# Kernel optimization log

Measured on AMD Instinct MI355X. Metric: run time of the kernel, lower is better.

## Reference

```python
import jax, jax.numpy as jnp
import numpy as np

MIN_NEAR = 0.05
DENSITY_SCALE = 1.0
BOUND = 1.0  # spherical scene bounds radius
GEO = 15


def _density_mlp(x, dW1, db1, dW2, db2, dW3, db3):
    h = jax.nn.relu(x @ dW1 + db1)
    h = jax.nn.relu(h @ dW2 + db2)
    h = h @ dW3 + db3  # [M, 1+GEO]
    sigma = jnp.exp(jnp.clip(h[..., 0], -15.0, 15.0))  # trunc_exp
    return sigma, h[..., 1:]


def _color_mlp(d, geo, cW1, cb1, cW2, cb2, cW3, cb3):
    h = jnp.concatenate([d, geo], axis=-1)
    h = jax.nn.relu(h @ cW1 + cb1)
    h = jax.nn.relu(h @ cW2 + cb2)
    return jax.nn.sigmoid(h @ cW3 + cb3)


def _comp_weights(deltas, sigmas):
    # alpha compositing: w_i = alpha_i * prod_{j<i}(1 - alpha_j)
    alphas = 1.0 - jnp.exp(-deltas * sigmas)
    trans = jnp.cumprod(
        jnp.concatenate([jnp.ones_like(alphas[:, :1]), 1.0 - alphas + 1e-15], axis=-1),
        axis=-1)[:, :-1]
    return alphas * trans


def _sample_pdf(bins, weights, n_samples):
    # deterministic importance resampling (eval mode); bins [N,T-1], weights [N,T-2]
    weights = weights + 1e-5
    pdf = weights / jnp.sum(weights, axis=-1, keepdims=True)
    cdf = jnp.cumsum(pdf, axis=-1)
    cdf = jnp.concatenate([jnp.zeros_like(cdf[:, :1]), cdf], axis=-1)  # [N, T-1]
    u = jnp.linspace(0.5 / n_samples, 1.0 - 0.5 / n_samples, n_samples)
    u = jnp.broadcast_to(u, (bins.shape[0], n_samples))
    inds = jax.vmap(lambda c, uu: jnp.searchsorted(c, uu, side='right'))(cdf, u)
    below = jnp.clip(inds - 1, 0, cdf.shape[-1] - 1)
    above = jnp.clip(inds, 0, cdf.shape[-1] - 1)
    cdf_g0 = jnp.take_along_axis(cdf, below, axis=-1)
    cdf_g1 = jnp.take_along_axis(cdf, above, axis=-1)
    bmax = bins.shape[-1] - 1
    bins_g0 = jnp.take_along_axis(bins, jnp.clip(below, 0, bmax), axis=-1)
    bins_g1 = jnp.take_along_axis(bins, jnp.clip(above, 0, bmax), axis=-1)
    denom = jnp.where(cdf_g1 - cdf_g0 < 1e-5, 1.0, cdf_g1 - cdf_g0)
    t = (u - cdf_g0) / denom
    return bins_g0 + t * (bins_g1 - bins_g0)


def _run(rays_o, rays_d, dW1, db1, dW2, db2, dW3, db3,
         cW1, cb1, cW2, cb2, cW3, cb3, num_steps, upsample_steps):
    N = rays_o.shape[0]
    # get_z_val_bounds: ray/sphere intersection, sphere radius BOUND at origin
    b = jnp.sum(rays_o * rays_d, axis=-1)
    c = jnp.sum(rays_o * rays_o, axis=-1) - BOUND ** 2
    disc = jnp.maximum(b * b - c, 0.0)
    z_max = jnp.maximum(-b + jnp.sqrt(disc), MIN_NEAR + 1e-3)
    z_min = jnp.full_like(z_max, MIN_NEAR)
    # get_foreground_z_vals: per-ray linspace (perturb=False)
    t = jnp.linspace(0.0, 1.0, num_steps)
    z_vals = z_min[:, None] + (z_max - z_min)[:, None] * t[None, :]
    z_vals = jnp.clip(z_vals, z_min[:, None], z_max[:, None])
    xyzs = rays_o[:, None, :] + rays_d[:, None, :] * z_vals[..., None]
    sigma, geo = _density_mlp(xyzs.reshape(-1, 3), dW1, db1, dW2, db2, dW3, db3)
    sigma = sigma.reshape(N, num_steps)
    geo = geo.reshape(N, num_steps, GEO)

    # upsample_z_values: importance resampling from coarse weights
    deltas = z_vals[:, 1:] - z_vals[:, :-1]
    aug = jnp.concatenate([deltas, deltas[:, -1:]], axis=-1)
    w_coarse = _comp_weights(aug, DENSITY_SCALE * sigma)
    z_mid = 0.5 * (z_vals[:, :-1] + z_vals[:, 1:])
    new_z = jax.lax.stop_gradient(_sample_pdf(z_mid, w_coarse[:, 1:-1], upsample_steps))
    new_xyzs = rays_o[:, None, :] + rays_d[:, None, :] * new_z[..., None]
    new_sigma, new_geo = _density_mlp(new_xyzs.reshape(-1, 3), dW1, db1, dW2, db2, dW3, db3)
    new_sigma = new_sigma.reshape(N, upsample_steps)
    new_geo = new_geo.reshape(N, upsample_steps, GEO)

    # sort/gather merge of coarse + fine samples
    z_all = jnp.concatenate([z_vals, new_z], axis=1)
    order = jnp.argsort(z_all, axis=1)
    z_vals = jnp.take_along_axis(z_all, order, axis=1)  # [N, T]
    xyzs = jnp.take_along_axis(jnp.concatenate([xyzs, new_xyzs], axis=1), order[..., None], axis=1)
    sigma = jnp.take_along_axis(jnp.concatenate([sigma, new_sigma], axis=1), order, axis=1)
    geo = jnp.take_along_axis(jnp.concatenate([geo, new_geo], axis=1), order[..., None], axis=1)

    deltas = z_vals[:, 1:] - z_vals[:, :-1]
    aug = jnp.concatenate([deltas, deltas[:, -1:]], axis=-1)
    weights = _comp_weights(aug, DENSITY_SCALE * sigma)  # [N, T]

    mask = weights > 1e-4
    dirs = jnp.broadcast_to(rays_d[:, None, :], xyzs.shape).reshape(-1, 3)
    rgb = _color_mlp(dirs, geo.reshape(-1, GEO), cW1, cb1, cW2, cb2, cW3, cb3)
    rgbs = jnp.where(mask.reshape(-1, 1), rgb, 0.0).reshape(N, -1, 3)

    weights_sum = jnp.sum(weights, axis=-1)
    depth = jnp.sum(weights * z_vals, axis=-1)
    image = jnp.sum(weights[..., None] * rgbs, axis=-2)
    bg = 206.0 / 255.0
    image = image + (1.0 - weights_sum)[..., None] * bg

    # pairwise distortion loss (the (z_shifted - z_shifted) term in the source is identically zero)
    sample_dist = 1.0 / num_steps
    z_shift = jnp.concatenate([z_vals[:, 1:], jnp.full((N, 1), sample_dist, z_vals.dtype)], axis=-1)
    mid_zs = 0.5 * z_vals + 0.5 * z_shift
    pair = jnp.abs(mid_zs[:, None, :] - mid_zs[:, :, None]) * (weights[:, None, :] * weights[:, :, None])
    loss = jnp.sum(pair, axis=(1, 2)) / (depth + 1e-6)
    loss = jnp.where(loss < 1e-3, 0.0, loss)  # cutoff
    return jnp.concatenate([image, depth[:, None], loss[:, None]], axis=-1)  # [N, 5]


def setup_inputs() -> dict:
    key = jax.random.key(0)
    ks = jax.random.split(key, 16)
    N, H = 2048, 256
    rays_o = 0.1 * jax.random.normal(ks[0], (N, 3), jnp.float32)  # near scene centre
    rd = jax.random.normal(ks[1], (N, 3), jnp.float32)
    rays_d = rd / jnp.linalg.norm(rd, axis=-1, keepdims=True)

    def w(k, shape):
        return jax.random.normal(k, shape, jnp.float32) * (1.0 / np.sqrt(shape[0]))

    return {
        'rays_o': rays_o, 'rays_d': rays_d,
        'dW1': w(ks[2], (3, H)), 'db1': jnp.zeros(H, jnp.float32),
        'dW2': w(ks[3], (H, H)), 'db2': jnp.zeros(H, jnp.float32),
        'dW3': w(ks[4], (H, 1 + GEO)), 'db3': jnp.zeros(1 + GEO, jnp.float32),
        'cW1': w(ks[5], (3 + GEO, H)), 'cb1': jnp.zeros(H, jnp.float32),
        'cW2': w(ks[6], (H, H)), 'cb2': jnp.zeros(H, jnp.float32),
        'cW3': w(ks[7], (H, 3)), 'cb3': jnp.zeros(3, jnp.float32),
        'num_steps': 128, 'upsample_steps': 128,
    }


def reference(rays_o, rays_d, dW1, db1, dW2, db2, dW3, db3,
              cW1, cb1, cW2, cb2, cW3, cb3, num_steps, upsample_steps):
    return _run(rays_o, rays_d, dW1, db1, dW2, db2, dW3, db3,
                cW1, cb1, cW2, cb2, cW3, cb3, num_steps, upsample_steps)
```

## Files before the change

kernel.cpp:

```cpp
#include <hip/hip_runtime.h>


typedef float f32x4 __attribute__((ext_vector_type(4)));
typedef __bf16 bf16x8 __attribute__((ext_vector_type(8)));
typedef unsigned short u16x8 __attribute__((ext_vector_type(8)));
typedef unsigned short u16x4 __attribute__((ext_vector_type(4)));

#define NRAYS 2048
#define NSTEP 128
#define TSAMP 256
#define MIN_NEAR 0.05f
#define DTPW 4
#define CTPW 4

__device__ __forceinline__ unsigned short f2bf(float f) {
  unsigned int u = __float_as_uint(f);
  u += 0x7FFFu + ((u >> 16) & 1u);
  return (unsigned short)(u >> 16);
}

__global__ void k_pack(const float* __restrict__ W, unsigned short* __restrict__ dst,
                       int K, int Norig, int NT, int total) {
  int idx = blockIdx.x * 256 + threadIdx.x;
  if (idx >= total) return;
  int per = NT * 512;
  int kt = idx / per;
  int rm = idx % per;
  int nt = rm >> 9;
  int lane = (rm >> 3) & 63;
  int j = rm & 7;
  int k = kt * 32 + ((lane >> 4) << 3) + j;
  int n = nt * 16 + (lane & 15);
  float v = (k < K && n < Norig) ? W[k * Norig + n] : 0.0f;
  dst[idx] = f2bf(v);
}

__global__ void k_pack_d3(const float* __restrict__ dW3, unsigned short* __restrict__ dst) {
  int idx = blockIdx.x * 256 + threadIdx.x;
  int lane = (idx >> 3) & 63;
  int j = idx & 7;
  int kt = idx >> 9;
  int k = kt * 32 + ((lane >> 4) << 3) + j;
  int n = lane & 15;
  dst[idx] = f2bf(dW3[k * 16 + ((n + 1) & 15)]);
}

__global__ void k_pack_c1(const float* __restrict__ cW1, unsigned short* __restrict__ dst) {
  int idx = blockIdx.x * 256 + threadIdx.x;
  int nt = idx >> 9;
  int lane = (idx >> 3) & 63;
  int j = idx & 7;
  int k = ((lane >> 4) << 3) + j;
  int n = nt * 16 + (lane & 15);
  float v = 0.0f;
  if (k < 15) v = cW1[(3 + k) * 256 + n];
  else if (k >= 16 && k < 19) v = cW1[(k - 16) * 256 + n];
  dst[idx] = f2bf(v);
}

__global__ void k_raysetup(const float* __restrict__ o, const float* __restrict__ d,
                           float* __restrict__ z_c) {
  int r = blockIdx.x, i = threadIdx.x;
  float ox = o[r * 3], oy = o[r * 3 + 1], oz = o[r * 3 + 2];
  float dx = d[r * 3], dy = d[r * 3 + 1], dz = d[r * 3 + 2];
  float b = ox * dx + oy * dy + oz * dz;
  float c = ox * ox + oy * oy + oz * oz - 1.0f;
  float disc = fmaxf(b * b - c, 0.0f);
  float zmax = fmaxf(-b + sqrtf(disc), MIN_NEAR + 1e-3f);
  float zmin = MIN_NEAR;
  float t = (float)i / 127.0f;
  float z = zmin + (zmax - zmin) * t;
  z = fminf(fmaxf(z, zmin), zmax);
  z_c[r * NSTEP + i] = z;
}


__device__ __forceinline__ void mlp_l1(const unsigned short* xb, unsigned short* buf,
                                       const bf16x8 (&w1r)[4], const float* sb1,
                                       int wid, int quad, int col) {
#pragma unroll
  for (int h = 0; h < 2; ++h) {
    f32x4 acc[8];
#pragma unroll
    for (int i = 0; i < 8; ++i) acc[i] = (f32x4){0.f, 0.f, 0.f, 0.f};
    int p0 = (h * 2) * 16 + col, p1 = (h * 2 + 1) * 16 + col;
    bf16x8 x0 = *reinterpret_cast<const bf16x8*>(&xb[p0 * 32 + ((quad ^ (p0 & 3)) * 8)]);
    bf16x8 x1 = *reinterpret_cast<const bf16x8*>(&xb[p1 * 32 + ((quad ^ (p1 & 3)) * 8)]);
#pragma unroll
    for (int ntl = 0; ntl < 4; ++ntl) {
      acc[ntl * 2 + 0] = __builtin_amdgcn_mfma_f32_16x16x32_bf16(w1r[ntl], x0, acc[ntl * 2 + 0], 0, 0, 0);
      acc[ntl * 2 + 1] = __builtin_amdgcn_mfma_f32_16x16x32_bf16(w1r[ntl], x1, acc[ntl * 2 + 1], 0, 0, 0);
    }
#pragma unroll
    for (int ntl = 0; ntl < 4; ++ntl) {
      int n = (wid * 4 + ntl) * 16 + quad * 4;
      f32x4 bv = *reinterpret_cast<const f32x4*>(&sb1[n]);
#pragma unroll
      for (int j = 0; j < 2; ++j) {
        int p = (h * 2 + j) * 16 + col;
        u16x4 pk;
#pragma unroll
        for (int rr = 0; rr < 4; ++rr)
          pk[rr] = f2bf(fmaxf(acc[ntl * 2 + j][rr] + bv[rr], 0.0f));
        *reinterpret_cast<u16x4*>(&buf[p * 256 + (((n >> 3) ^ (p & 31)) * 8) + (n & 7)]) = pk;
      }
    }
  }
}

__device__ __forceinline__ void l2_half_compute(const unsigned short* buf,
                                                const bf16x8 (&w2r)[8][4],
                                                f32x4 (&acc)[8], int h, int quad, int col) {
#pragma unroll
  for (int i = 0; i < 8; ++i) acc[i] = (f32x4){0.f, 0.f, 0.f, 0.f};
#pragma unroll
  for (int kt = 0; kt < 8; ++kt) {
    int p0 = (h * 2) * 16 + col, p1 = (h * 2 + 1) * 16 + col;
    bf16x8 x0 = *reinterpret_cast<const bf16x8*>(&buf[p0 * 256 + (((kt * 4 + quad) ^ (p0 & 31)) * 8)]);
    bf16x8 x1 = *reinterpret_cast<const bf16x8*>(&buf[p1 * 256 + (((kt * 4 + quad) ^ (p1 & 31)) * 8)]);
#pragma unroll
    for (int ntl = 0; ntl < 4; ++ntl) {
      acc[ntl * 2 + 0] = __builtin_amdgcn_mfma_f32_16x16x32_bf16(w2r[kt][ntl], x0, acc[ntl * 2 + 0], 0, 0, 0);
      acc[ntl * 2 + 1] = __builtin_amdgcn_mfma_f32_16x16x32_bf16(w2r[kt][ntl], x1, acc[ntl * 2 + 1], 0, 0, 0);
    }
  }
}

__device__ __forceinline__ void l2_half_write(unsigned short* buf, const f32x4 (&acc)[8],
                                              const float* sb2, int h, int wid, int quad, int col) {
#pragma unroll
  for (int ntl = 0; ntl < 4; ++ntl) {
    int n = (wid * 4 + ntl) * 16 + quad * 4;
    f32x4 bv = *reinterpret_cast<const f32x4*>(&sb2[n]);
#pragma unroll
    for (int j = 0; j < 2; ++j) {
      int p = (h * 2 + j) * 16 + col;
      u16x4 pk;
#pragma unroll
      for (int rr = 0; rr < 4; ++rr)
        pk[rr] = f2bf(fmaxf(acc[ntl * 2 + j][rr] + bv[rr], 0.0f));
      *reinterpret_cast<u16x4*>(&buf[p * 256 + (((n >> 3) ^ (p & 31)) * 8) + (n & 7)]) = pk;
    }
  }
}

__global__ __launch_bounds__(256, 2)
void k_density(const float* __restrict__ rays_o, const float* __restrict__ rays_d,
               const float* __restrict__ z,
               const unsigned short* __restrict__ Wp1, const float* __restrict__ b1,
               const unsigned short* __restrict__ Wp2, const float* __restrict__ b2,
               const unsigned short* __restrict__ Wp3, const float* __restrict__ b3,
               unsigned short* __restrict__ gout, float* __restrict__ sig) {
  __shared__ unsigned short buf[64 * 256];
  __shared__ unsigned short xb[64 * 32];
  __shared__ unsigned short sW3[4096];
  __shared__ __align__(16) float sb1[256];
  __shared__ __align__(16) float sb2[256];
  __shared__ float sb3[16];
  const int t = threadIdx.x;
  const int lane = t & 63, wid = t >> 6, quad = lane >> 4, col = lane & 15;
  const int p_ = t >> 2, g_ = t & 3;

  sb1[t] = b1[t];
  sb2[t] = b2[t];
  if (t < 16) sb3[t] = b3[(t + 1) & 15];
  { const u16x8* s = (const u16x8*)Wp3; u16x8* d = (u16x8*)sW3;
    d[t] = s[t]; d[t + 256] = s[t + 256]; }

  bf16x8 w1r[4], w2r[8][4];
#pragma unroll
  for (int ntl = 0; ntl < 4; ++ntl)
    w1r[ntl] = *reinterpret_cast<const bf16x8*>(Wp1 + ((wid * 4 + ntl) * 64 + lane) * 8);
#pragma unroll
  for (int kt = 0; kt < 8; ++kt)
#pragma unroll
    for (int ntl = 0; ntl < 4; ++ntl)
      w2r[kt][ntl] = *reinterpret_cast<const bf16x8*>(Wp2 + ((kt * 16 + wid * 4 + ntl) * 64 + lane) * 8);

  float zv = z[blockIdx.x * DTPW * 64 + p_];

#pragma unroll 1
  for (int tt = 0; tt < DTPW; ++tt) {
    const int P0 = (blockIdx.x * DTPW + tt) * 64;
    {
      u16x8 pk = {0, 0, 0, 0, 0, 0, 0, 0};
      if (g_ == 0) {
        int r = (P0 + p_) >> 7;
        pk[0] = f2bf(rays_o[r * 3 + 0] + rays_d[r * 3 + 0] * zv);
        pk[1] = f2bf(rays_o[r * 3 + 1] + rays_d[r * 3 + 1] * zv);
        pk[2] = f2bf(rays_o[r * 3 + 2] + rays_d[r * 3 + 2] * zv);
      }
      *reinterpret_cast<u16x8*>(&xb[p_ * 32 + ((g_ ^ (p_ & 3)) * 8)]) = pk;
    }
    __syncthreads();
    mlp_l1(xb, buf, w1r, sb1, wid, quad, col);
    __syncthreads();
    float zn = 0.0f;
    if (tt + 1 < DTPW) zn = z[P0 + 64 + p_];
    f32x4 acc[8];
    l2_half_compute(buf, w2r, acc, 0, quad, col);
    __syncthreads();
    l2_half_write(buf, acc, sb2, 0, wid, quad, col);
    l2_half_compute(buf, w2r, acc, 1, quad, col);
    __syncthreads();
    l2_half_write(buf, acc, sb2, 1, wid, quad, col);
    __syncthreads();
    {
      const int p = wid * 16 + col;
      f32x4 a3 = {0.f, 0.f, 0.f, 0.f};
#pragma unroll
      for (int kt = 0; kt < 8; ++kt) {
        bf16x8 w = *reinterpret_cast<const bf16x8*>(&sW3[(kt * 64 + lane) * 8]);
        bf16x8 x = *reinterpret_cast<const bf16x8*>(&buf[p * 256 + (((kt * 4 + quad) ^ (p & 31)) * 8)]);
        a3 = __builtin_amdgcn_mfma_f32_16x16x32_bf16(w, x, a3, 0, 0, 0);
      }
      int n0 = quad * 4;
      u16x4 pk;
#pragma unroll
      for (int rr = 0; rr < 4; ++rr) {
        float v = a3[rr] + sb3[n0 + rr];
        if (quad == 3 && rr == 3) {
          sig[P0 + p] = expf(fminf(fmaxf(v, -15.f), 15.f));
          pk[rr] = 0;
        } else {
          pk[rr] = f2bf(v);
        }
      }
      *reinterpret_cast<u16x4*>(gout + (size_t)(P0 + p) * 16 + n0) = pk;
    }
    zv = zn;
  }
}

__global__ void k_pdf(const float* __restrict__ z_c, const float* __restrict__ sigc,
                      float* __restrict__ z_f) {
  __shared__ float sz[128], sl[128], sw[128], scdf[128], szmid[128];
  int r = blockIdx.x, i = threadIdx.x;
  float zi = z_c[r * NSTEP + i];
  sz[i] = zi;
  float sg = sigc[r * NSTEP + i];
  __syncthreads();
  float aug = (i < 127) ? (sz[i + 1] - zi) : (sz[127] - sz[126]);
  float alpha = 1.0f - expf(-aug * sg);
  float term = 1.0f - alpha + 1e-15f;
  sl[i] = logf(term);
  __syncthreads();
  for (int off = 1; off < 128; off <<= 1) {
    float y = (i >= off) ? sl[i - off] : 0.0f;
    __syncthreads();
    sl[i] += y;
    __syncthreads();
  }
  float excl = (i > 0) ? sl[i - 1] : 0.0f;
  float w = alpha * expf(excl);
  sw[i] = w;
  __syncthreads();
  float v = (i < 126) ? (sw[i + 1] + 1e-5f) : 0.0f;
  sl[i] = v;
  __syncthreads();
  for (int off = 1; off < 128; off <<= 1) {
    float y = (i >= off) ? sl[i - off] : 0.0f;
    __syncthreads();
    sl[i] += y;
    __syncthreads();
  }
  float total = sl[125];
  if (i <= 126) scdf[i] = (i == 0) ? 0.0f : sl[i - 1] / total;
  if (i < 127) szmid[i] = 0.5f * (sz[i] + sz[i + 1]);
  __syncthreads();
  const float lo = 0.5f / 128.0f, hi = 1.0f - 0.5f / 128.0f;
  float u = lo + (hi - lo) * ((float)i / 127.0f);
  int loI = 0, hiI = 127;
  while (loI < hiI) {
    int mid = (loI + hiI) >> 1;
    if (scdf[mid] > u) hiI = mid; else loI = mid + 1;
  }
  int inds = loI;
  int below = inds - 1; if (below < 0) below = 0; if (below > 126) below = 126;
  int above = inds; if (above > 126) above = 126;
  float c0 = scdf[below], c1 = scdf[above];
  float b0 = szmid[below], b1 = szmid[above];
  float dn = c1 - c0; if (dn < 1e-5f) dn = 1.0f;
  float tt = (u - c0) / dn;
  z_f[r * NSTEP + i] = b0 + tt * (b1 - b0);
}

__global__ void k_merge(const float* __restrict__ z_c, const float* __restrict__ z_f,
                        const float* __restrict__ sigc, const float* __restrict__ sigf,
                        float* __restrict__ z_m, int* __restrict__ order,
                        float* __restrict__ wgt) {
  __shared__ float szc[128], szf[128], szm[256], sl[256];
  __shared__ int sord[256];
  int r = blockIdx.x, t = threadIdx.x;
  if (t < 128) szc[t] = z_c[r * NSTEP + t];
  else szf[t - 128] = z_f[r * NSTEP + t - 128];
  __syncthreads();
  int pos; float myz;
  if (t < 128) {
    myz = szc[t];
    int lo = 0, hi = 128;
    while (lo < hi) { int m = (lo + hi) >> 1; if (szf[m] < myz) lo = m + 1; else hi = m; }
    pos = t + lo;
  } else {
    int j = t - 128; myz = szf[j];
    int lo = 0, hi = 128;
    while (lo < hi) { int m = (lo + hi) >> 1; if (szc[m] <= myz) lo = m + 1; else hi = m; }
    pos = j + lo;
  }
  szm[pos] = myz; sord[pos] = t;
  __syncthreads();
  z_m[r * TSAMP + t] = szm[t];
  order[r * TSAMP + t] = sord[t];
  int src = sord[t];
  float sg = (src < 128) ? sigc[r * NSTEP + src] : sigf[r * NSTEP + (src - 128)];
  float zt = szm[t];
  float aug = (t < 255) ? (szm[t + 1] - zt) : (szm[255] - szm[254]);
  float alpha = 1.0f - expf(-aug * sg);
  sl[t] = logf(1.0f - alpha + 1e-15f);
  __syncthreads();
  for (int off = 1; off < 256; off <<= 1) {
    float y = (t >= off) ? sl[t - off] : 0.0f;
    __syncthreads();
    sl[t] += y;
    __syncthreads();
  }
  float excl = (t > 0) ? sl[t - 1] : 0.0f;
  wgt[r * TSAMP + t] = alpha * expf(excl);
}

__global__ __launch_bounds__(256, 2)
void k_color(const float* __restrict__ rays_d, const int* __restrict__ order,
             const float* __restrict__ wgt,
             const unsigned short* __restrict__ goutc, const unsigned short* __restrict__ goutf,
             const unsigned short* __restrict__ Wp1, const float* __restrict__ cb1,
             const unsigned short* __restrict__ Wp2, const float* __restrict__ cb2,
             const unsigned short* __restrict__ Wp3, const float* __restrict__ cb3,
             float* __restrict__ rgb4) {
  __shared__ unsigned short buf[64 * 256];
  __shared__ unsigned short xb[64 * 32];
  __shared__ unsigned short sW3[4096];
  __shared__ __align__(16) float sb1[256];
  __shared__ __align__(16) float sb2[256];
  const int t = threadIdx.x;
  const int lane = t & 63, wid = t >> 6, quad = lane >> 4, col = lane & 15;
  const int p_ = t >> 2, g_ = t & 3;

  sb1[t] = cb1[t];
  sb2[t] = cb2[t];
  { const u16x8* s = (const u16x8*)Wp3; u16x8* d = (u16x8*)sW3;
    d[t] = s[t]; d[t + 256] = s[t + 256]; }

  bf16x8 w1r[4], w2r[8][4];
#pragma unroll
  for (int ntl = 0; ntl < 4; ++ntl)
    w1r[ntl] = *reinterpret_cast<const bf16x8*>(Wp1 + ((wid * 4 + ntl) * 64 + lane) * 8);
#pragma unroll
  for (int kt = 0; kt < 8; ++kt)
#pragma unroll
    for (int ntl = 0; ntl < 4; ++ntl)
      w2r[kt][ntl] = *reinterpret_cast<const bf16x8*>(Wp2 + ((kt * 16 + wid * 4 + ntl) * 64 + lane) * 8);

  u16x8 gx = {0, 0, 0, 0, 0, 0, 0, 0};
  float wgtv = 0.0f;
  {
    int P = blockIdx.x * CTPW * 64 + p_;
    int r = P >> 8;
    if (g_ < 2) {
      int src = order[P];
      const unsigned short* gs = (src < 128)
          ? (goutc + (size_t)(r * NSTEP + src) * 16)
          : (goutf + (size_t)(r * NSTEP + (src - 128)) * 16);
      gx = *reinterpret_cast<const u16x8*>(gs + g_ * 8);
    } else if (g_ == 2) {
      gx[0] = f2bf(rays_d[r * 3 + 0]);
      gx[1] = f2bf(rays_d[r * 3 + 1]);
      gx[2] = f2bf(rays_d[r * 3 + 2]);
    } else {
      wgtv = wgt[P];
    }
  }

#pragma unroll 1
  for (int tt = 0; tt < CTPW; ++tt) {
    const int P0 = (blockIdx.x * CTPW + tt) * 64;
    const int haveNext = (tt + 1 < CTPW);
    int go = __syncthreads_or((g_ == 3) && (wgtv > 1e-4f));
    int ordn = 0; float wgtn = 0.0f;
    u16x8 gxn = {0, 0, 0, 0, 0, 0, 0, 0};
    if (go) {
      *reinterpret_cast<u16x8*>(&xb[p_ * 32 + ((g_ ^ (p_ & 3)) * 8)]) = gx;
      __syncthreads();
      mlp_l1(xb, buf, w1r, sb1, wid, quad, col);
      __syncthreads();
    }
    if (haveNext) {
      int Pn = P0 + 64 + p_;
      int rn = Pn >> 8;
      if (g_ < 2) ordn = order[Pn];
      else if (g_ == 2) {
        gxn[0] = f2bf(rays_d[rn * 3 + 0]);
        gxn[1] = f2bf(rays_d[rn * 3 + 1]);
        gxn[2] = f2bf(rays_d[rn * 3 + 2]);
      } else wgtn = wgt[Pn];
    }
    f32x4 acc[8];
    if (go) {
      l2_half_compute(buf, w2r, acc, 0, quad, col);
      __syncthreads();
      l2_half_write(buf, acc, sb2, 0, wid, quad, col);
    }
    if (haveNext && g_ < 2) {
      int Pn = P0 + 64 + p_;
      int rn = Pn >> 8;
      const unsigned short* gs = (ordn < 128)
          ? (goutc + (size_t)(rn * NSTEP + ordn) * 16)
          : (goutf + (size_t)(rn * NSTEP + (ordn - 128)) * 16);
      gxn = *reinterpret_cast<const u16x8*>(gs + g_ * 8);
    }
    if (go) {
      l2_half_compute(buf, w2r, acc, 1, quad, col);
      __syncthreads();
      l2_half_write(buf, acc, sb2, 1, wid, quad, col);
      __syncthreads();
      {
        const int p = wid * 16 + col;
        f32x4 a3 = {0.f, 0.f, 0.f, 0.f};
#pragma unroll
        for (int kt = 0; kt < 8; ++kt) {
          bf16x8 w = *reinterpret_cast<const bf16x8*>(&sW3[(kt * 64 + lane) * 8]);
          bf16x8 x = *reinterpret_cast<const bf16x8*>(&buf[p * 256 + (((kt * 4 + quad) ^ (p & 31)) * 8)]);
          a3 = __builtin_amdgcn_mfma_f32_16x16x32_bf16(w, x, a3, 0, 0, 0);
        }
        if (quad == 0) {
          f32x4 v;
#pragma unroll
          for (int rr = 0; rr < 3; ++rr) {
            float s = a3[rr] + cb3[rr];
            v[rr] = 1.0f / (1.0f + expf(-s));
          }
          v[3] = 0.0f;
          *reinterpret_cast<f32x4*>(rgb4 + (size_t)(P0 + p) * 4) = v;
        }
      }
    }
    gx = gxn; wgtv = wgtn;
  }
}

__device__ __forceinline__ float block_reduce(float v, float* s, int t) {
  s[t] = v;
  __syncthreads();
  for (int off = 128; off > 0; off >>= 1) {
    if (t < off) s[t] += s[t + off];
    __syncthreads();
  }
  float r = s[0];
  __syncthreads();
  return r;
}

__global__ void k_final(const float* __restrict__ z_m, const float* __restrict__ wgt,
                        const float* __restrict__ rgb4, float* __restrict__ out) {
  __shared__ float sz[256], sw[256], smid[256], sred[256];
  int r = blockIdx.x, t = threadIdx.x;
  float zt = z_m[r * TSAMP + t];
  float wt = wgt[r * TSAMP + t];
  sz[t] = zt; sw[t] = wt;
  __syncthreads();
  float znext = (t < 255) ? sz[t + 1] : (1.0f / 128.0f);
  smid[t] = 0.5f * zt + 0.5f * znext;
  float cr = 0.f, cg = 0.f, cb = 0.f;
  if (wt > 1e-4f) {
    f32x4 c = *reinterpret_cast<const f32x4*>(rgb4 + (size_t)(r * TSAMP + t) * 4);
    cr = c[0]; cg = c[1]; cb = c[2];
  }
  __syncthreads();
  float mt = smid[t];
  float acc = 0.f;
  for (int j = 0; j < 256; ++j) acc += fabsf(mt - smid[j]) * sw[j];
  acc *= wt;
  float wsum = block_reduce(wt, sred, t);
  float depth = block_reduce(wt * zt, sred, t);
  float ir = block_reduce(wt * cr, sred, t);
  float ig = block_reduce(wt * cg, sred, t);
  float ib = block_reduce(wt * cb, sred, t);
  float S = block_reduce(acc, sred, t);
  if (t == 0) {
    const float bgc = 206.0f / 255.0f;
    float loss = S / (depth + 1e-6f);
    if (loss < 1e-3f) loss = 0.0f;
    out[r * 5 + 0] = ir + (1.0f - wsum) * bgc;
    out[r * 5 + 1] = ig + (1.0f - wsum) * bgc;
    out[r * 5 + 2] = ib + (1.0f - wsum) * bgc;
    out[r * 5 + 3] = depth;
    out[r * 5 + 4] = loss;
  }
}

extern "C" void kernel_launch(void* const* d_in, const int* in_sizes, int n_in,
                              void* d_out, int out_size, void* d_ws, size_t ws_size,
                              hipStream_t stream) {
  const float* rays_o = (const float*)d_in[0];
  const float* rays_d = (const float*)d_in[1];
  const float* dW1 = (const float*)d_in[2];
  const float* db1 = (const float*)d_in[3];
  const float* dW2 = (const float*)d_in[4];
  const float* db2 = (const float*)d_in[5];
  const float* dW3 = (const float*)d_in[6];
  const float* db3 = (const float*)d_in[7];
  const float* cW1 = (const float*)d_in[8];
  const float* cb1 = (const float*)d_in[9];
  const float* cW2 = (const float*)d_in[10];
  const float* cb2 = (const float*)d_in[11];
  const float* cW3 = (const float*)d_in[12];
  const float* cb3 = (const float*)d_in[13];

  char* ws = (char*)d_ws;
  size_t off = 0;
  auto alloc = [&](size_t bytes) -> void* {
    void* p = ws + off;
    off += (bytes + 255) & ~(size_t)255;
    return p;
  };
  unsigned short* Wp_d1 = (unsigned short*)alloc(8192 * 2);
  unsigned short* Wp_d2 = (unsigned short*)alloc(65536 * 2);
  unsigned short* Wp_d3 = (unsigned short*)alloc(4096 * 2);
  unsigned short* Wp_c1 = (unsigned short*)alloc(8192 * 2);
  unsigned short* Wp_c2 = (unsigned short*)alloc(65536 * 2);
  unsigned short* Wp_c3 = (unsigned short*)alloc(4096 * 2);
  float* z_c  = (float*)alloc((size_t)NRAYS * NSTEP * 4);
  float* z_f  = (float*)alloc((size_t)NRAYS * NSTEP * 4);
  unsigned short* goutc = (unsigned short*)alloc((size_t)NRAYS * NSTEP * 16 * 2);
  unsigned short* goutf = (unsigned short*)alloc((size_t)NRAYS * NSTEP * 16 * 2);
  float* sigc = (float*)alloc((size_t)NRAYS * NSTEP * 4);
  float* sigf = (float*)alloc((size_t)NRAYS * NSTEP * 4);
  float* z_m  = (float*)alloc((size_t)NRAYS * TSAMP * 4);
  int*   ordr = (int*)alloc((size_t)NRAYS * TSAMP * 4);
  float* wgt  = (float*)alloc((size_t)NRAYS * TSAMP * 4);
  float* rgb4 = (float*)alloc((size_t)NRAYS * TSAMP * 4 * 4);
  (void)ws_size; (void)in_sizes; (void)n_in; (void)out_size;

  k_pack<<<8192 / 256, 256, 0, stream>>>(dW1, Wp_d1, 3, 256, 16, 8192);
  k_pack<<<65536 / 256, 256, 0, stream>>>(dW2, Wp_d2, 256, 256, 16, 65536);
  k_pack_d3<<<4096 / 256, 256, 0, stream>>>(dW3, Wp_d3);
  k_pack_c1<<<8192 / 256, 256, 0, stream>>>(cW1, Wp_c1);
  k_pack<<<65536 / 256, 256, 0, stream>>>(cW2, Wp_c2, 256, 256, 16, 65536);
  k_pack<<<4096 / 256, 256, 0, stream>>>(cW3, Wp_c3, 256, 3, 1, 4096);

  k_raysetup<<<NRAYS, 128, 0, stream>>>(rays_o, rays_d, z_c);
  k_density<<<(NRAYS * NSTEP) / (64 * DTPW), 256, 0, stream>>>(
      rays_o, rays_d, z_c, Wp_d1, db1, Wp_d2, db2, Wp_d3, db3, goutc, sigc);
  k_pdf<<<NRAYS, 128, 0, stream>>>(z_c, sigc, z_f);
  k_density<<<(NRAYS * NSTEP) / (64 * DTPW), 256, 0, stream>>>(
      rays_o, rays_d, z_f, Wp_d1, db1, Wp_d2, db2, Wp_d3, db3, goutf, sigf);
  k_merge<<<NRAYS, 256, 0, stream>>>(z_c, z_f, sigc, sigf, z_m, ordr, wgt);
  k_color<<<(NRAYS * TSAMP) / (64 * CTPW), 256, 0, stream>>>(
      rays_d, ordr, wgt, goutc, goutf, Wp_c1, cb1, Wp_c2, cb2, Wp_c3, cb3, rgb4);
  k_final<<<NRAYS, 256, 0, stream>>>(z_m, wgt, rgb4, (float*)d_out);
}
```

Baseline: 308.9 us.

## Fuse pack, raysetup, pdf, merge, color and final passes into fewer kernels

Merges the six weight-pack kernels into one launch and computes the coarse z values inline instead of in a separate setup kernel. The PDF resampling now runs at the end of the first density pass, since each 256-point block covers exactly two rays. Merge, color MLP and final compositing become one per-ray kernel that keeps order, weights and rgb in shared memory rather than global memory. This cuts launches and global round-trips, but the color kernel now runs with one ray per block, loads its weights into registers per ray, and uses more shared memory, which may lower occupancy.

```diff
diff --git a/kernel.cpp b/kernel.cpp
--- a/kernel.cpp
+++ b/kernel.cpp
@@ -3,6 +3,7 @@
 
 typedef float f32x4 __attribute__((ext_vector_type(4)));
 typedef __bf16 bf16x8 __attribute__((ext_vector_type(8)));
+typedef __bf16 bf16x4 __attribute__((ext_vector_type(4)));
 typedef unsigned short u16x8 __attribute__((ext_vector_type(8)));
 typedef unsigned short u16x4 __attribute__((ext_vector_type(4)));
 
@@ -11,67 +12,80 @@
 #define TSAMP 256
 #define MIN_NEAR 0.05f
 #define DTPW 4
-#define CTPW 4
+
+#define OFF_D1 0
+#define OFF_D2 8192
+#define OFF_D3 73728
+#define OFF_C1 77824
+#define OFF_C2 86016
+#define OFF_C3 151552
+#define PACK_TOTAL 155648
 
 __device__ __forceinline__ unsigned short f2bf(float f) {
-  unsigned int u = __float_as_uint(f);
-  u += 0x7FFFu + ((u >> 16) & 1u);
-  return (unsigned short)(u >> 16);
-}
-
-__global__ void k_pack(const float* __restrict__ W, unsigned short* __restrict__ dst,
-                       int K, int Norig, int NT, int total) {
-  int idx = blockIdx.x * 256 + threadIdx.x;
-  if (idx >= total) return;
-  int per = NT * 512;
-  int kt = idx / per;
-  int rm = idx % per;
-  int nt = rm >> 9;
-  int lane = (rm >> 3) & 63;
-  int j = rm & 7;
-  int k = kt * 32 + ((lane >> 4) << 3) + j;
-  int n = nt * 16 + (lane & 15);
-  float v = (k < K && n < Norig) ? W[k * Norig + n] : 0.0f;
-  dst[idx] = f2bf(v);
-}
-
-__global__ void k_pack_d3(const float* __restrict__ dW3, unsigned short* __restrict__ dst) {
-  int idx = blockIdx.x * 256 + threadIdx.x;
-  int lane = (idx >> 3) & 63;
-  int j = idx & 7;
-  int kt = idx >> 9;
-  int k = kt * 32 + ((lane >> 4) << 3) + j;
-  int n = lane & 15;
-  dst[idx] = f2bf(dW3[k * 16 + ((n + 1) & 15)]);
-}
-
-__global__ void k_pack_c1(const float* __restrict__ cW1, unsigned short* __restrict__ dst) {
-  int idx = blockIdx.x * 256 + threadIdx.x;
-  int nt = idx >> 9;
-  int lane = (idx >> 3) & 63;
-  int j = idx & 7;
-  int k = ((lane >> 4) << 3) + j;
-  int n = nt * 16 + (lane & 15);
-  float v = 0.0f;
-  if (k < 15) v = cW1[(3 + k) * 256 + n];
-  else if (k >= 16 && k < 19) v = cW1[(k - 16) * 256 + n];
-  dst[idx] = f2bf(v);
-}
-
-__global__ void k_raysetup(const float* __restrict__ o, const float* __restrict__ d,
-                           float* __restrict__ z_c) {
-  int r = blockIdx.x, i = threadIdx.x;
-  float ox = o[r * 3], oy = o[r * 3 + 1], oz = o[r * 3 + 2];
-  float dx = d[r * 3], dy = d[r * 3 + 1], dz = d[r * 3 + 2];
+  __bf16 h = (__bf16)f;
+  return __builtin_bit_cast(unsigned short, h);
+}
+__device__ __forceinline__ u16x4 pack4(float a, float b, float c, float d) {
+  bf16x4 h;
+  h[0] = (__bf16)a; h[1] = (__bf16)b; h[2] = (__bf16)c; h[3] = (__bf16)d;
+  return __builtin_bit_cast(u16x4, h);
+}
+
+__device__ __forceinline__ float ray_z(const float* __restrict__ ro,
+                                       const float* __restrict__ rd, int r, int i) {
+  float ox = ro[r * 3], oy = ro[r * 3 + 1], oz = ro[r * 3 + 2];
+  float dx = rd[r * 3], dy = rd[r * 3 + 1], dz = rd[r * 3 + 2];
   float b = ox * dx + oy * dy + oz * dz;
   float c = ox * ox + oy * oy + oz * oz - 1.0f;
   float disc = fmaxf(b * b - c, 0.0f);
   float zmax = fmaxf(-b + sqrtf(disc), MIN_NEAR + 1e-3f);
   float zmin = MIN_NEAR;
-  float t = (float)i / 127.0f;
-  float z = zmin + (zmax - zmin) * t;
-  z = fminf(fmaxf(z, zmin), zmax);
-  z_c[r * NSTEP + i] = z;
+  float tt = (float)i / 127.0f;
+  float zz = zmin + (zmax - zmin) * tt;
+  return fminf(fmaxf(zz, zmin), zmax);
+}
+
+__device__ __forceinline__ void pack_std(const float* __restrict__ W,
+                                         unsigned short* __restrict__ dst,
+                                         int idx, int K, int Norig, int NT) {
+  int per = NT * 512;
+  int kt = idx / per, rm = idx % per;
+  int nt = rm >> 9, lane = (rm >> 3) & 63, j = rm & 7;
+  int k = kt * 32 + ((lane >> 4) << 3) + j;
+  int n = nt * 16 + (lane & 15);
+  float v = (k < K && n < Norig) ? W[k * Norig + n] : 0.0f;
+  dst[idx] = f2bf(v);
+}
+
+__global__ void k_pack_all(const float* __restrict__ dW1, const float* __restrict__ dW2,
+                           const float* __restrict__ dW3, const float* __restrict__ cW1,
+                           const float* __restrict__ cW2, const float* __restrict__ cW3,
+                           unsigned short* __restrict__ Wp) {
+  int idx = blockIdx.x * 256 + threadIdx.x;
+  if (idx < OFF_D2) {
+    pack_std(dW1, Wp + OFF_D1, idx - OFF_D1, 3, 256, 16);
+  } else if (idx < OFF_D3) {
+    pack_std(dW2, Wp + OFF_D2, idx - OFF_D2, 256, 256, 16);
+  } else if (idx < OFF_C1) {
+    int j2 = idx - OFF_D3;
+    int lane = (j2 >> 3) & 63, jj = j2 & 7, kt = j2 >> 9;
+    int k = kt * 32 + ((lane >> 4) << 3) + jj;
+    int n = lane & 15;
+    Wp[idx] = f2bf(dW3[k * 16 + ((n + 1) & 15)]);
+  } else if (idx < OFF_C2) {
+    int j2 = idx - OFF_C1;
+    int nt = j2 >> 9, lane = (j2 >> 3) & 63, jj = j2 & 7;
+    int k = ((lane >> 4) << 3) + jj;
+    int n = nt * 16 + (lane & 15);
+    float v = 0.0f;
+    if (k < 15) v = cW1[(3 + k) * 256 + n];
+    else if (k >= 16 && k < 19) v = cW1[(k - 16) * 256 + n];
+    Wp[idx] = f2bf(v);
+  } else if (idx < OFF_C3) {
+    pack_std(cW2, Wp + OFF_C2, idx - OFF_C2, 256, 256, 16);
+  } else if (idx < PACK_TOTAL) {
+    pack_std(cW3, Wp + OFF_C3, idx - OFF_C3, 256, 3, 1);
+  }
 }
 
 
@@ -98,11 +112,11 @@
 #pragma unroll
       for (int j = 0; j < 2; ++j) {
         int p = (h * 2 + j) * 16 + col;
-        u16x4 pk;
-#pragma unroll
-        for (int rr = 0; rr < 4; ++rr)
-          pk[rr] = f2bf(fmaxf(acc[ntl * 2 + j][rr] + bv[rr], 0.0f));
-        *reinterpret_cast<u16x4*>(&buf[p * 256 + (((n >> 3) ^ (p & 31)) * 8) + (n & 7)]) = pk;
+        *reinterpret_cast<u16x4*>(&buf[p * 256 + (((n >> 3) ^ (p & 31)) * 8) + (n & 7)]) =
+            pack4(fmaxf(acc[ntl * 2 + j][0] + bv[0], 0.0f),
+                  fmaxf(acc[ntl * 2 + j][1] + bv[1], 0.0f),
+                  fmaxf(acc[ntl * 2 + j][2] + bv[2], 0.0f),
+                  fmaxf(acc[ntl * 2 + j][3] + bv[3], 0.0f));
       }
     }
   }
@@ -135,28 +149,31 @@
 #pragma unroll
     for (int j = 0; j < 2; ++j) {
       int p = (h * 2 + j) * 16 + col;
-      u16x4 pk;
-#pragma unroll
-      for (int rr = 0; rr < 4; ++rr)
-        pk[rr] = f2bf(fmaxf(acc[ntl * 2 + j][rr] + bv[rr], 0.0f));
-      *reinterpret_cast<u16x4*>(&buf[p * 256 + (((n >> 3) ^ (p & 31)) * 8) + (n & 7)]) = pk;
-    }
-  }
-}
-
+      *reinterpret_cast<u16x4*>(&buf[p * 256 + (((n >> 3) ^ (p & 31)) * 8) + (n & 7)]) =
+          pack4(fmaxf(acc[ntl * 2 + j][0] + bv[0], 0.0f),
+                fmaxf(acc[ntl * 2 + j][1] + bv[1], 0.0f),
+                fmaxf(acc[ntl * 2 + j][2] + bv[2], 0.0f),
+                fmaxf(acc[ntl * 2 + j][3] + bv[3], 0.0f));
+    }
+  }
+}
+
+template <bool FIRST>
 __global__ __launch_bounds__(256, 2)
-void k_density(const float* __restrict__ rays_o, const float* __restrict__ rays_d,
-               const float* __restrict__ z,
+void k_density(const float* __restrict__ ro, const float* __restrict__ rd,
+               const float* __restrict__ zin,
                const unsigned short* __restrict__ Wp1, const float* __restrict__ b1,
                const unsigned short* __restrict__ Wp2, const float* __restrict__ b2,
                const unsigned short* __restrict__ Wp3, const float* __restrict__ b3,
-               unsigned short* __restrict__ gout, float* __restrict__ sig) {
-  __shared__ unsigned short buf[64 * 256];
+               unsigned short* __restrict__ gout, float* __restrict__ sig,
+               float* __restrict__ z_f) {
+  __shared__ __align__(16) unsigned short buf[64 * 256];
   __shared__ unsigned short xb[64 * 32];
   __shared__ unsigned short sW3[4096];
   __shared__ __align__(16) float sb1[256];
   __shared__ __align__(16) float sb2[256];
   __shared__ float sb3[16];
+  __shared__ float ssig[256];
   const int t = threadIdx.x;
   const int lane = t & 63, wid = t >> 6, quad = lane >> 4, col = lane & 15;
   const int p_ = t >> 2, g_ = t & 3;
@@ -177,26 +194,26 @@
     for (int ntl = 0; ntl < 4; ++ntl)
       w2r[kt][ntl] = *reinterpret_cast<const bf16x8*>(Wp2 + ((kt * 16 + wid * 4 + ntl) * 64 + lane) * 8);
 
-  float zv = z[blockIdx.x * DTPW * 64 + p_];
-
 #pragma unroll 1
   for (int tt = 0; tt < DTPW; ++tt) {
-    const int P0 = (blockIdx.x * DTPW + tt) * 64;
+    const int P0 = blockIdx.x * 256 + tt * 64;
     {
       u16x8 pk = {0, 0, 0, 0, 0, 0, 0, 0};
       if (g_ == 0) {
-        int r = (P0 + p_) >> 7;
-        pk[0] = f2bf(rays_o[r * 3 + 0] + rays_d[r * 3 + 0] * zv);
-        pk[1] = f2bf(rays_o[r * 3 + 1] + rays_d[r * 3 + 1] * zv);
-        pk[2] = f2bf(rays_o[r * 3 + 2] + rays_d[r * 3 + 2] * zv);
+        int P = P0 + p_;
+        int rr_ = P >> 7, ii = P & 127;
+        float zz;
+        if constexpr (FIRST) zz = ray_z(ro, rd, rr_, ii);
+        else zz = zin[P];
+        pk[0] = f2bf(ro[rr_ * 3 + 0] + rd[rr_ * 3 + 0] * zz);
+        pk[1] = f2bf(ro[rr_ * 3 + 1] + rd[rr_ * 3 + 1] * zz);
+        pk[2] = f2bf(ro[rr_ * 3 + 2] + rd[rr_ * 3 + 2] * zz);
       }
       *reinterpret_cast<u16x8*>(&xb[p_ * 32 + ((g_ ^ (p_ & 3)) * 8)]) = pk;
     }
     __syncthreads();
     mlp_l1(xb, buf, w1r, sb1, wid, quad, col);
     __syncthreads();
-    float zn = 0.0f;
-    if (tt + 1 < DTPW) zn = z[P0 + 64 + p_];
     f32x4 acc[8];
     l2_half_compute(buf, w2r, acc, 0, quad, col);
     __syncthreads();
@@ -215,85 +232,127 @@
         a3 = __builtin_amdgcn_mfma_f32_16x16x32_bf16(w, x, a3, 0, 0, 0);
       }
       int n0 = quad * 4;
-      u16x4 pk;
-#pragma unroll
-      for (int rr = 0; rr < 4; ++rr) {
-        float v = a3[rr] + sb3[n0 + rr];
-        if (quad == 3 && rr == 3) {
-          sig[P0 + p] = expf(fminf(fmaxf(v, -15.f), 15.f));
-          pk[rr] = 0;
-        } else {
-          pk[rr] = f2bf(v);
-        }
+      float v0 = a3[0] + sb3[n0], v1 = a3[1] + sb3[n0 + 1];
+      float v2 = a3[2] + sb3[n0 + 2], v3 = a3[3] + sb3[n0 + 3];
+      if (quad == 3) {
+        float sgm = expf(fminf(fmaxf(v3, -15.f), 15.f));
+        sig[P0 + p] = sgm;
+        ssig[tt * 64 + p] = sgm;
+        v3 = 0.0f;
       }
-      *reinterpret_cast<u16x4*>(gout + (size_t)(P0 + p) * 16 + n0) = pk;
-    }
-    zv = zn;
-  }
-}
-
-__global__ void k_pdf(const float* __restrict__ z_c, const float* __restrict__ sigc,
-                      float* __restrict__ z_f) {
-  __shared__ float sz[128], sl[128], sw[128], scdf[128], szmid[128];
-  int r = blockIdx.x, i = threadIdx.x;
-  float zi = z_c[r * NSTEP + i];
-  sz[i] = zi;
-  float sg = sigc[r * NSTEP + i];
-  __syncthreads();
-  float aug = (i < 127) ? (sz[i + 1] - zi) : (sz[127] - sz[126]);
-  float alpha = 1.0f - expf(-aug * sg);
-  float term = 1.0f - alpha + 1e-15f;
-  sl[i] = logf(term);
-  __syncthreads();
-  for (int off = 1; off < 128; off <<= 1) {
-    float y = (i >= off) ? sl[i - off] : 0.0f;
-    __syncthreads();
-    sl[i] += y;
-    __syncthreads();
-  }
-  float excl = (i > 0) ? sl[i - 1] : 0.0f;
-  float w = alpha * expf(excl);
-  sw[i] = w;
-  __syncthreads();
-  float v = (i < 126) ? (sw[i + 1] + 1e-5f) : 0.0f;
-  sl[i] = v;
-  __syncthreads();
-  for (int off = 1; off < 128; off <<= 1) {
-    float y = (i >= off) ? sl[i - off] : 0.0f;
-    __syncthreads();
-    sl[i] += y;
-    __syncthreads();
-  }
-  float total = sl[125];
-  if (i <= 126) scdf[i] = (i == 0) ? 0.0f : sl[i - 1] / total;
-  if (i < 127) szmid[i] = 0.5f * (sz[i] + sz[i + 1]);
-  __syncthreads();
-  const float lo = 0.5f / 128.0f, hi = 1.0f - 0.5f / 128.0f;
-  float u = lo + (hi - lo) * ((float)i / 127.0f);
-  int loI = 0, hiI = 127;
-  while (loI < hiI) {
-    int mid = (loI + hiI) >> 1;
-    if (scdf[mid] > u) hiI = mid; else loI = mid + 1;
-  }
-  int inds = loI;
-  int below = inds - 1; if (below < 0) below = 0; if (below > 126) below = 126;
-  int above = inds; if (above > 126) above = 126;
-  float c0 = scdf[below], c1 = scdf[above];
-  float b0 = szmid[below], b1 = szmid[above];
-  float dn = c1 - c0; if (dn < 1e-5f) dn = 1.0f;
-  float tt = (u - c0) / dn;
-  z_f[r * NSTEP + i] = b0 + tt * (b1 - b0);
-}
-
-__global__ void k_merge(const float* __restrict__ z_c, const float* __restrict__ z_f,
-                        const float* __restrict__ sigc, const float* __restrict__ sigf,
-                        float* __restrict__ z_m, int* __restrict__ order,
-                        float* __restrict__ wgt) {
-  __shared__ float szc[128], szf[128], szm[256], sl[256];
+      *reinterpret_cast<u16x4*>(gout + (size_t)(P0 + p) * 16 + n0) = pack4(v0, v1, v2, v3);
+    }
+  }
+
+  if constexpr (FIRST) {
+    __syncthreads();
+    float* pf = reinterpret_cast<float*>(buf);
+    float* psz = pf;          float* psl = pf + 256;
+    float* psw = pf + 512;    float* pcdf = pf + 768;
+    float* pmid = pf + 1024;
+    const int seg = (t >> 7) * 128;
+    const int i = t & 127;
+    const int rg = blockIdx.x * 2 + (t >> 7);
+    float zi = ray_z(ro, rd, rg, i);
+    psz[seg + i] = zi;
+    float sgv = ssig[t];
+    __syncthreads();
+    float aug = (i < 127) ? psz[seg + i + 1] - zi : psz[seg + 127] - psz[seg + 126];
+    float alpha = 1.0f - expf(-aug * sgv);
+    psl[seg + i] = logf(1.0f - alpha + 1e-15f);
+    __syncthreads();
+    for (int off = 1; off < 128; off <<= 1) {
+      float y = (i >= off) ? psl[seg + i - off] : 0.0f;
+      __syncthreads();
+      psl[seg + i] += y;
+      __syncthreads();
+    }
+    float excl = (i > 0) ? psl[seg + i - 1] : 0.0f;
+    float w = alpha * expf(excl);
+    psw[seg + i] = w;
+    __syncthreads();
+    float v = (i < 126) ? psw[seg + i + 1] + 1e-5f : 0.0f;
+    psl[seg + i] = v;
+    __syncthreads();
+    for (int off = 1; off < 128; off <<= 1) {
+      float y = (i >= off) ? psl[seg + i - off] : 0.0f;
+      __syncthreads();
+      psl[seg + i] += y;
+      __syncthreads();
+    }
+    float total = psl[seg + 125];
+    if (i <= 126) pcdf[seg + i] = (i == 0) ? 0.0f : psl[seg + i - 1] / total;
+    if (i < 127) pmid[seg + i] = 0.5f * (psz[seg + i] + psz[seg + i + 1]);
+    __syncthreads();
+    const float lo = 0.5f / 128.0f, hi = 1.0f - 0.5f / 128.0f;
+    float u = lo + (hi - lo) * ((float)i / 127.0f);
+    int loI = 0, hiI = 127;
+    while (loI < hiI) {
+      int mid = (loI + hiI) >> 1;
+      if (pcdf[seg + mid] > u) hiI = mid; else loI = mid + 1;
+    }
+    int below = loI - 1; if (below < 0) below = 0; if (below > 126) below = 126;
+    int above = loI;     if (above > 126) above = 126;
+    float c0 = pcdf[seg + below], c1 = pcdf[seg + above];
+    float b0v = pmid[seg + below], b1v = pmid[seg + above];
+    float dn = c1 - c0; if (dn < 1e-5f) dn = 1.0f;
+    float ttt = (u - c0) / dn;
+    z_f[rg * NSTEP + i] = b0v + ttt * (b1v - b0v);
+  }
+}
+
+__device__ __forceinline__ float block_reduce(float v, float* s, int t) {
+  s[t] = v;
+  __syncthreads();
+  for (int off = 128; off > 0; off >>= 1) {
+    if (t < off) s[t] += s[t + off];
+    __syncthreads();
+  }
+  float r = s[0];
+  __syncthreads();
+  return r;
+}
+
+__global__ __launch_bounds__(256, 2)
+void k_mcf(const float* __restrict__ ro, const float* __restrict__ rd,
+           const float* __restrict__ z_f,
+           const float* __restrict__ sigc, const float* __restrict__ sigf,
+           const unsigned short* __restrict__ goutc, const unsigned short* __restrict__ goutf,
+           const unsigned short* __restrict__ Wp1, const float* __restrict__ cb1,
+           const unsigned short* __restrict__ Wp2, const float* __restrict__ cb2,
+           const unsigned short* __restrict__ Wp3, const float* __restrict__ cb3,
+           float* __restrict__ out) {
+  __shared__ __align__(16) unsigned short buf[64 * 256];
+  __shared__ unsigned short xb[64 * 32];
+  __shared__ unsigned short sW3[4096];
+  __shared__ __align__(16) float sb1[256];
+  __shared__ __align__(16) float sb2[256];
+  __shared__ float szm[256], swgt[256], smid[256], sred[256], sl[256];
+  __shared__ float szc[128], szf[128];
+  __shared__ float srgb[3 * 256];
   __shared__ int sord[256];
-  int r = blockIdx.x, t = threadIdx.x;
-  if (t < 128) szc[t] = z_c[r * NSTEP + t];
-  else szf[t - 128] = z_f[r * NSTEP + t - 128];
+  const int t = threadIdx.x;
+  const int lane = t & 63, wid = t >> 6, quad = lane >> 4, col = lane & 15;
+  const int p_ = t >> 2, g_ = t & 3;
+  const int r = blockIdx.x;
+
+  sb1[t] = cb1[t];
+  sb2[t] = cb2[t];
+  { const u16x8* s = (const u16x8*)Wp3; u16x8* d = (u16x8*)sW3;
+    d[t] = s[t]; d[t + 256] = s[t + 256]; }
+
+  bf16x8 w1r[4], w2r[8][4];
+#pragma unroll
+  for (int ntl = 0; ntl < 4; ++ntl)
+    w1r[ntl] = *reinterpret_cast<const bf16x8*>(Wp1 + ((wid * 4 + ntl) * 64 + lane) * 8);
+#pragma unroll
+  for (int kt = 0; kt < 8; ++kt)
+#pragma unroll
+    for (int ntl = 0; ntl < 4; ++ntl)
+      w2r[kt][ntl] = *reinterpret_cast<const bf16x8*>(Wp2 + ((kt * 16 + wid * 4 + ntl) * 64 + lane) * 8);
+
+  if (t < 128) szc[t] = ray_z(ro, rd, r, t);
+  else szf[t - 128] = z_f[r * NSTEP + (t - 128)];
   __syncthreads();
   int pos; float myz;
   if (t < 128) {
@@ -309,12 +368,10 @@
   }
   szm[pos] = myz; sord[pos] = t;
   __syncthreads();
-  z_m[r * TSAMP + t] = szm[t];
-  order[r * TSAMP + t] = sord[t];
   int src = sord[t];
   float sg = (src < 128) ? sigc[r * NSTEP + src] : sigf[r * NSTEP + (src - 128)];
   float zt = szm[t];
-  float aug = (t < 255) ? (szm[t + 1] - zt) : (szm[255] - szm[254]);
+  float aug = (t < 255) ? szm[t + 1] - zt : szm[255] - szm[254];
   float alpha = 1.0f - expf(-aug * sg);
   sl[t] = logf(1.0f - alpha + 1e-15f);
   __syncthreads();
@@ -325,68 +382,32 @@
     __syncthreads();
   }
   float excl = (t > 0) ? sl[t - 1] : 0.0f;
-  wgt[r * TSAMP + t] = alpha * expf(excl);
-}
-
-__global__ __launch_bounds__(256, 2)
-void k_color(const float* __restrict__ rays_d, const int* __restrict__ order,
-             const float* __restrict__ wgt,
-             const unsigned short* __restrict__ goutc, const unsigned short* __restrict__ goutf,
-             const unsigned short* __restrict__ Wp1, const float* __restrict__ cb1,
-             const unsigned short* __restrict__ Wp2, const float* __restrict__ cb2,
-             const unsigned short* __restrict__ Wp3, const float* __restrict__ cb3,
-             float* __restrict__ rgb4) {
-  __shared__ unsigned short buf[64 * 256];
-  __shared__ unsigned short xb[64 * 32];
-  __shared__ unsigned short sW3[4096];
-  __shared__ __align__(16) float sb1[256];
-  __shared__ __align__(16) float sb2[256];
-  const int t = threadIdx.x;
-  const int lane = t & 63, wid = t >> 6, quad = lane >> 4, col = lane & 15;
-  const int p_ = t >> 2, g_ = t & 3;
-
-  sb1[t] = cb1[t];
-  sb2[t] = cb2[t];
-  { const u16x8* s = (const u16x8*)Wp3; u16x8* d = (u16x8*)sW3;
-    d[t] = s[t]; d[t + 256] = s[t + 256]; }
-
-  bf16x8 w1r[4], w2r[8][4];
-#pragma unroll
-  for (int ntl = 0; ntl < 4; ++ntl)
-    w1r[ntl] = *reinterpret_cast<const bf16x8*>(Wp1 + ((wid * 4 + ntl) * 64 + lane) * 8);
-#pragma unroll
-  for (int kt = 0; kt < 8; ++kt)
-#pragma unroll
-    for (int ntl = 0; ntl < 4; ++ntl)
-      w2r[kt][ntl] = *reinterpret_cast<const bf16x8*>(Wp2 + ((kt * 16 + wid * 4 + ntl) * 64 + lane) * 8);
-
+  swgt[t] = alpha * expf(excl);
+
+  float dx0 = rd[r * 3], dx1 = rd[r * 3 + 1], dx2 = rd[r * 3 + 2];
+  __syncthreads();
   u16x8 gx = {0, 0, 0, 0, 0, 0, 0, 0};
   float wgtv = 0.0f;
   {
-    int P = blockIdx.x * CTPW * 64 + p_;
-    int r = P >> 8;
     if (g_ < 2) {
-      int src = order[P];
-      const unsigned short* gs = (src < 128)
-          ? (goutc + (size_t)(r * NSTEP + src) * 16)
-          : (goutf + (size_t)(r * NSTEP + (src - 128)) * 16);
+      int s0 = sord[p_];
+      const unsigned short* gs = (s0 < 128)
+          ? (goutc + (size_t)(r * NSTEP + s0) * 16)
+          : (goutf + (size_t)(r * NSTEP + (s0 - 128)) * 16);
       gx = *reinterpret_cast<const u16x8*>(gs + g_ * 8);
     } else if (g_ == 2) {
-      gx[0] = f2bf(rays_d[r * 3 + 0]);
-      gx[1] = f2bf(rays_d[r * 3 + 1]);
-      gx[2] = f2bf(rays_d[r * 3 + 2]);
+      gx[0] = f2bf(dx0); gx[1] = f2bf(dx1); gx[2] = f2bf(dx2);
     } else {
-      wgtv = wgt[P];
-    }
-  }
-
+      wgtv = swgt[p_];
+    }
+  }
 #pragma unroll 1
-  for (int tt = 0; tt < CTPW; ++tt) {
-    const int P0 = (blockIdx.x * CTPW + tt) * 64;
-    const int haveNext = (tt + 1 < CTPW);
+  for (int tt = 0; tt < 4; ++tt) {
+    const int P0l = tt * 64;
+    const int haveNext = (tt < 3);
     int go = __syncthreads_or((g_ == 3) && (wgtv > 1e-4f));
-    int ordn = 0; float wgtn = 0.0f;
     u16x8 gxn = {0, 0, 0, 0, 0, 0, 0, 0};
+    float wgtn = 0.0f; int ordn = 0;
     if (go) {
       *reinterpret_cast<u16x8*>(&xb[p_ * 32 + ((g_ ^ (p_ & 3)) * 8)]) = gx;
       __syncthreads();
@@ -394,14 +415,10 @@
       __syncthreads();
     }
     if (haveNext) {
-      int Pn = P0 + 64 + p_;
-      int rn = Pn >> 8;
-      if (g_ < 2) ordn = order[Pn];
-      else if (g_ == 2) {
-        gxn[0] = f2bf(rays_d[rn * 3 + 0]);
-        gxn[1] = f2bf(rays_d[rn * 3 + 1]);
-        gxn[2] = f2bf(rays_d[rn * 3 + 2]);
-      } else wgtn = wgt[Pn];
+      int Pn = P0l + 64 + p_;
+      if (g_ < 2) ordn = sord[Pn];
+      else if (g_ == 2) { gxn[0] = f2bf(dx0); gxn[1] = f2bf(dx1); gxn[2] = f2bf(dx2); }
+      else wgtn = swgt[Pn];
     }
     f32x4 acc[8];
     if (go) {
@@ -410,11 +427,9 @@
       l2_half_write(buf, acc, sb2, 0, wid, quad, col);
     }
     if (haveNext && g_ < 2) {
-      int Pn = P0 + 64 + p_;
-      int rn = Pn >> 8;
       const unsigned short* gs = (ordn < 128)
-          ? (goutc + (size_t)(rn * NSTEP + ordn) * 16)
-          : (goutf + (size_t)(rn * NSTEP + (ordn - 128)) * 16);
+          ? (goutc + (size_t)(r * NSTEP + ordn) * 16)
+          : (goutf + (size_t)(r * NSTEP + (ordn - 128)) * 16);
       gxn = *reinterpret_cast<const u16x8*>(gs + g_ * 8);
     }
     if (go) {
@@ -432,59 +447,35 @@
           a3 = __builtin_amdgcn_mfma_f32_16x16x32_bf16(w, x, a3, 0, 0, 0);
         }
         if (quad == 0) {
-          f32x4 v;
-#pragma unroll
-          for (int rr = 0; rr < 3; ++rr) {
-            float s = a3[rr] + cb3[rr];
-            v[rr] = 1.0f / (1.0f + expf(-s));
-          }
-          v[3] = 0.0f;
-          *reinterpret_cast<f32x4*>(rgb4 + (size_t)(P0 + p) * 4) = v;
+          int pi = P0l + p;
+          srgb[pi * 3 + 0] = 1.0f / (1.0f + expf(-(a3[0] + cb3[0])));
+          srgb[pi * 3 + 1] = 1.0f / (1.0f + expf(-(a3[1] + cb3[1])));
+          srgb[pi * 3 + 2] = 1.0f / (1.0f + expf(-(a3[2] + cb3[2])));
         }
       }
     }
     gx = gxn; wgtv = wgtn;
   }
-}
-
-__device__ __forceinline__ float block_reduce(float v, float* s, int t) {
-  s[t] = v;
-  __syncthreads();
-  for (int off = 128; off > 0; off >>= 1) {
-    if (t < off) s[t] += s[t + off];
-    __syncthreads();
-  }
-  float r = s[0];
-  __syncthreads();
-  return r;
-}
-
-__global__ void k_final(const float* __restrict__ z_m, const float* __restrict__ wgt,
-                        const float* __restrict__ rgb4, float* __restrict__ out) {
-  __shared__ float sz[256], sw[256], smid[256], sred[256];
-  int r = blockIdx.x, t = threadIdx.x;
-  float zt = z_m[r * TSAMP + t];
-  float wt = wgt[r * TSAMP + t];
-  sz[t] = zt; sw[t] = wt;
-  __syncthreads();
-  float znext = (t < 255) ? sz[t + 1] : (1.0f / 128.0f);
-  smid[t] = 0.5f * zt + 0.5f * znext;
-  float cr = 0.f, cg = 0.f, cb = 0.f;
-  if (wt > 1e-4f) {
-    f32x4 c = *reinterpret_cast<const f32x4*>(rgb4 + (size_t)(r * TSAMP + t) * 4);
-    cr = c[0]; cg = c[1]; cb = c[2];
+
+  __syncthreads();
+  float ztf = szm[t], wtf = swgt[t];
+  float znext = (t < 255) ? szm[t + 1] : (1.0f / 128.0f);
+  smid[t] = 0.5f * ztf + 0.5f * znext;
+  float cr = 0.f, cg = 0.f, cbv = 0.f;
+  if (wtf > 1e-4f) {
+    cr = srgb[t * 3]; cg = srgb[t * 3 + 1]; cbv = srgb[t * 3 + 2];
   }
   __syncthreads();
   float mt = smid[t];
-  float acc = 0.f;
-  for (int j = 0; j < 256; ++j) acc += fabsf(mt - smid[j]) * sw[j];
-  acc *= wt;
-  float wsum = block_reduce(wt, sred, t);
-  float depth = block_reduce(wt * zt, sred, t);
-  float ir = block_reduce(wt * cr, sred, t);
-  float ig = block_reduce(wt * cg, sred, t);
-  float ib = block_reduce(wt * cb, sred, t);
-  float S = block_reduce(acc, sred, t);
+  float accl = 0.f;
+  for (int j = 0; j < 256; ++j) accl += fabsf(mt - smid[j]) * swgt[j];
+  accl *= wtf;
+  float wsum = block_reduce(wtf, sred, t);
+  float depth = block_reduce(wtf * ztf, sred, t);
+  float ir = block_reduce(wtf * cr, sred, t);
+  float ig = block_reduce(wtf * cg, sred, t);
+  float ib = block_reduce(wtf * cbv, sred, t);
+  float S = block_reduce(accl, sred, t);
   if (t == 0) {
     const float bgc = 206.0f / 255.0f;
     float loss = S / (depth + 1e-6f);
@@ -522,39 +513,23 @@
     off += (bytes + 255) & ~(size_t)255;
     return p;
   };
-  unsigned short* Wp_d1 = (unsigned short*)alloc(8192 * 2);
-  unsigned short* Wp_d2 = (unsigned short*)alloc(65536 * 2);
-  unsigned short* Wp_d3 = (unsigned short*)alloc(4096 * 2);
-  unsigned short* Wp_c1 = (unsigned short*)alloc(8192 * 2);
-  unsigned short* Wp_c2 = (unsigned short*)alloc(65536 * 2);
-  unsigned short* Wp_c3 = (unsigned short*)alloc(4096 * 2);
-  float* z_c  = (float*)alloc((size_t)NRAYS * NSTEP * 4);
-  float* z_f  = (float*)alloc((size_t)NRAYS * NSTEP * 4);
+  unsigned short* Wp = (unsigned short*)alloc((size_t)PACK_TOTAL * 2);
   unsigned short* goutc = (unsigned short*)alloc((size_t)NRAYS * NSTEP * 16 * 2);
   unsigned short* goutf = (unsigned short*)alloc((size_t)NRAYS * NSTEP * 16 * 2);
   float* sigc = (float*)alloc((size_t)NRAYS * NSTEP * 4);
   float* sigf = (float*)alloc((size_t)NRAYS * NSTEP * 4);
-  float* z_m  = (float*)alloc((size_t)NRAYS * TSAMP * 4);
-  int*   ordr = (int*)alloc((size_t)NRAYS * TSAMP * 4);
-  float* wgt  = (float*)alloc((size_t)NRAYS * TSAMP * 4);
-  float* rgb4 = (float*)alloc((size_t)NRAYS * TSAMP * 4 * 4);
+  float* z_f  = (float*)alloc((size_t)NRAYS * NSTEP * 4);
   (void)ws_size; (void)in_sizes; (void)n_in; (void)out_size;
 
-  k_pack<<<8192 / 256, 256, 0, stream>>>(dW1, Wp_d1, 3, 256, 16, 8192);
-  k_pack<<<65536 / 256, 256, 0, stream>>>(dW2, Wp_d2, 256, 256, 16, 65536);
-  k_pack_d3<<<4096 / 256, 256, 0, stream>>>(dW3, Wp_d3);
-  k_pack_c1<<<8192 / 256, 256, 0, stream>>>(cW1, Wp_c1);
-  k_pack<<<65536 / 256, 256, 0, stream>>>(cW2, Wp_c2, 256, 256, 16, 65536);
-  k_pack<<<4096 / 256, 256, 0, stream>>>(cW3, Wp_c3, 256, 3, 1, 4096);
-
-  k_raysetup<<<NRAYS, 128, 0, stream>>>(rays_o, rays_d, z_c);
-  k_density<<<(NRAYS * NSTEP) / (64 * DTPW), 256, 0, stream>>>(
-      rays_o, rays_d, z_c, Wp_d1, db1, Wp_d2, db2, Wp_d3, db3, goutc, sigc);
-  k_pdf<<<NRAYS, 128, 0, stream>>>(z_c, sigc, z_f);
-  k_density<<<(NRAYS * NSTEP) / (64 * DTPW), 256, 0, stream>>>(
-      rays_o, rays_d, z_f, Wp_d1, db1, Wp_d2, db2, Wp_d3, db3, goutf, sigf);
-  k_merge<<<NRAYS, 256, 0, stream>>>(z_c, z_f, sigc, sigf, z_m, ordr, wgt);
-  k_color<<<(NRAYS * TSAMP) / (64 * CTPW), 256, 0, stream>>>(
-      rays_d, ordr, wgt, goutc, goutf, Wp_c1, cb1, Wp_c2, cb2, Wp_c3, cb3, rgb4);
-  k_final<<<NRAYS, 256, 0, stream>>>(z_m, wgt, rgb4, (float*)d_out);
-}
+  k_pack_all<<<PACK_TOTAL / 256, 256, 0, stream>>>(dW1, dW2, dW3, cW1, cW2, cW3, Wp);
+
+  k_density<true><<<(NRAYS * NSTEP) / 256, 256, 0, stream>>>(
+      rays_o, rays_d, nullptr,
+      Wp + OFF_D1, db1, Wp + OFF_D2, db2, Wp + OFF_D3, db3, goutc, sigc, z_f);
+  k_density<false><<<(NRAYS * NSTEP) / 256, 256, 0, stream>>>(
+      rays_o, rays_d, z_f,
+      Wp + OFF_D1, db1, Wp + OFF_D2, db2, Wp + OFF_D3, db3, goutf, sigf, nullptr);
+  k_mcf<<<NRAYS, 256, 0, stream>>>(
+      rays_o, rays_d, z_f, sigc, sigf, goutc, goutf,
+      Wp + OFF_C1, cb1, Wp + OFF_C2, cb2, Wp + OFF_C3, cb3, (float*)d_out);
+}
```

Measured after the change: 289.0 us. 6.4% less time.
